# Performance work log

Measured on AMD Instinct MI355X. Metric: run time of the kernel, lower is better.

## Reference

```python
import jax, jax.numpy as jnp
import numpy as np

B, O, R, I, D = 256, 10, 1152, 8, 16
NUM_ITERATIONS = 3


def squash(x, axis=-1):
    sq = jnp.sum(x * x, axis=axis, keepdims=True)
    return (sq / (1.0 + sq)) * x / jnp.sqrt(sq)


def setup_inputs() -> dict:
    key = jax.random.key(0)
    k1, k2 = jax.random.split(key)
    inputs = jax.random.normal(k1, (B, R, I), dtype=jnp.float32)
    route_weights = jax.random.normal(k2, (O, R, I, D), dtype=jnp.float32)
    return {"inputs": inputs, "route_weights": route_weights}


def reference(inputs, route_weights):
    # priors: [B, O, R, D]  (torch keeps an extra singleton dim: [B,O,R,1,D])
    priors = jnp.einsum('bri,orid->bord', inputs, route_weights)
    logits = jnp.zeros_like(priors)  # torch initializes logits with priors' shape
    outputs = None
    for _ in range(NUM_ITERATIONS):
        probs = jax.nn.softmax(logits, axis=2)  # softmax over route nodes (dim=2)
        outputs = squash(jnp.sum(probs * priors, axis=2, keepdims=True))  # [B,O,1,D]
        delta = jnp.sum(priors * outputs, axis=-1, keepdims=True)  # [B,O,R,1]
        logits = logits + delta  # broadcasts over vec dim, as in torch
    return outputs  # [B, O, 1, D]
```

## Files before the change

### kernel.cpp

```cpp
#include <hip/hip_runtime.h>


#define BB 256
#define OO 10
#define RR 1152
#define DD 16
#define NITER 3
#define NT 384
#define NB 2
#define GRID (OO * BB / NB)
#define NW 6

template<int CTRL>
__device__ __forceinline__ float dpp_add(float x) {
    int p = __builtin_amdgcn_update_dpp(0, __float_as_int(x), CTRL, 0xF, 0xF, true);
    return x + __int_as_float(p);
}
__device__ __forceinline__ float red_dq(float x) {
    x = dpp_add<0xB1>(x);
    x = dpp_add<0x4E>(x);
    return x;
}
__device__ __forceinline__ float4 fma4(float4 w, float a, float4 c) {
    c.x = fmaf(w.x, a, c.x); c.y = fmaf(w.y, a, c.y);
    c.z = fmaf(w.z, a, c.z); c.w = fmaf(w.w, a, c.w);
    return c;
}
__device__ __forceinline__ float dot4(float4 a, float4 b) {
    return fmaf(a.x, b.x, fmaf(a.y, b.y, fmaf(a.z, b.z, a.w * b.w)));
}
__device__ __forceinline__ float red_rs(float x) {
    x += __shfl_xor(x, 4);  x += __shfl_xor(x, 8);
    x += __shfl_xor(x, 16); x += __shfl_xor(x, 32);
    return x;
}
__device__ __forceinline__ float4 red_rs4(float4 v) {
    v.x = red_rs(v.x); v.y = red_rs(v.y); v.z = red_rs(v.z); v.w = red_rs(v.w);
    return v;
}

struct F4x4 { float4 q0, q1, q2, q3; };

__global__ void capsule_direct(
    const float* __restrict__ inp,
    const float* __restrict__ W,
    float* __restrict__ out)
{
    __shared__ float4 priB[12 * NT];
    __shared__ float4 red4[NB][NW][4];
    __shared__ float  redS[NB][NW];
    __shared__ __align__(16) float finalv[NB][20];

    int wg = blockIdx.x;
    wg = (wg & 7) * (GRID / 8) + (wg >> 3);
    const int o  = wg / (BB / NB);
    const int b0 = (wg % (BB / NB)) * NB;
    const int tid = threadIdx.x;
    const int dq = tid & 3;
    const int rslot = tid >> 2;
    const int wid = tid >> 6;
    const int lane = tid & 63;

    const float4* w4 = reinterpret_cast<const float4*>(W) + (size_t)o * (RR * 32) + dq;
    const float4* ip = reinterpret_cast<const float4*>(inp);

    F4x4 PAa{}, PAb{}, PAc{};
    float4 lgAa{0,0,0,0}, lgAb{0,0,0,0}, lgAc{0,0,0,0};
    float4 lgBa{0,0,0,0}, lgBb{0,0,0,0}, lgBc{0,0,0,0};

#define DO_C(C, PACC) do {                                                     \
        const int row_ = (C) * 96 + rslot;                                     \
        const float4 a0_ = ip[((size_t)b0 * RR + row_) * 2];                   \
        const float4 a1_ = ip[((size_t)b0 * RR + row_) * 2 + 1];               \
        const float4 c0_ = ip[((size_t)(b0 + 1) * RR + row_) * 2];             \
        const float4 c1_ = ip[((size_t)(b0 + 1) * RR + row_) * 2 + 1];         \
        const float4* wr_ = w4 + row_ * 32;                                    \
        float4 pb_{0.f, 0.f, 0.f, 0.f};                                        \
        float4 w_;                                                             \
        w_ = wr_[0];  PACC = fma4(w_, a0_.x, PACC); pb_ = fma4(w_, c0_.x, pb_);\
        w_ = wr_[4];  PACC = fma4(w_, a0_.y, PACC); pb_ = fma4(w_, c0_.y, pb_);\
        w_ = wr_[8];  PACC = fma4(w_, a0_.z, PACC); pb_ = fma4(w_, c0_.z, pb_);\
        w_ = wr_[12]; PACC = fma4(w_, a0_.w, PACC); pb_ = fma4(w_, c0_.w, pb_);\
        w_ = wr_[16]; PACC = fma4(w_, a1_.x, PACC); pb_ = fma4(w_, c1_.x, pb_);\
        w_ = wr_[20]; PACC = fma4(w_, a1_.y, PACC); pb_ = fma4(w_, c1_.y, pb_);\
        w_ = wr_[24]; PACC = fma4(w_, a1_.z, PACC); pb_ = fma4(w_, c1_.z, pb_);\
        w_ = wr_[28]; PACC = fma4(w_, a1_.w, PACC); pb_ = fma4(w_, c1_.w, pb_);\
        priB[(C) * NT + tid] = pb_;                                            \
    } while (0)

    DO_C(0,  PAa.q0); DO_C(1,  PAa.q1); DO_C(2,  PAa.q2); DO_C(3,  PAa.q3);
    DO_C(4,  PAb.q0); DO_C(5,  PAb.q1); DO_C(6,  PAb.q2); DO_C(7,  PAb.q3);
    DO_C(8,  PAc.q0); DO_C(9,  PAc.q1); DO_C(10, PAc.q2); DO_C(11, PAc.q3);

    #pragma unroll
    for (int it = 0; it < NITER; ++it) {
        {
            float4 ea, eb, ec;
            ea.x = __expf(lgAa.x); ea.y = __expf(lgAa.y);
            ea.z = __expf(lgAa.z); ea.w = __expf(lgAa.w);
            eb.x = __expf(lgAb.x); eb.y = __expf(lgAb.y);
            eb.z = __expf(lgAb.z); eb.w = __expf(lgAb.w);
            ec.x = __expf(lgAc.x); ec.y = __expf(lgAc.y);
            ec.z = __expf(lgAc.z); ec.w = __expf(lgAc.w);
            float Se = ea.x + ea.y + ea.z + ea.w + eb.x + eb.y + eb.z + eb.w
                     + ec.x + ec.y + ec.z + ec.w;
            float4 s4{0.f, 0.f, 0.f, 0.f};
            s4 = fma4(PAa.q0, ea.x, s4); s4 = fma4(PAa.q1, ea.y, s4);
            s4 = fma4(PAa.q2, ea.z, s4); s4 = fma4(PAa.q3, ea.w, s4);
            s4 = fma4(PAb.q0, eb.x, s4); s4 = fma4(PAb.q1, eb.y, s4);
            s4 = fma4(PAb.q2, eb.z, s4); s4 = fma4(PAb.q3, eb.w, s4);
            s4 = fma4(PAc.q0, ec.x, s4); s4 = fma4(PAc.q1, ec.y, s4);
            s4 = fma4(PAc.q2, ec.z, s4); s4 = fma4(PAc.q3, ec.w, s4);
            s4 = red_rs4(s4);
            Se = red_rs(Se);
            if (lane < 4) red4[0][wid][lane] = s4;
            else if (lane == 4) redS[0][wid] = Se;
        }
        {
            float4 ea, eb, ec;
            ea.x = __expf(lgBa.x); ea.y = __expf(lgBa.y);
            ea.z = __expf(lgBa.z); ea.w = __expf(lgBa.w);
            eb.x = __expf(lgBb.x); eb.y = __expf(lgBb.y);
            eb.z = __expf(lgBb.z); eb.w = __expf(lgBb.w);
            ec.x = __expf(lgBc.x); ec.y = __expf(lgBc.y);
            ec.z = __expf(lgBc.z); ec.w = __expf(lgBc.w);
            float Se = ea.x + ea.y + ea.z + ea.w + eb.x + eb.y + eb.z + eb.w
                     + ec.x + ec.y + ec.z + ec.w;
            float4 s4{0.f, 0.f, 0.f, 0.f};
            s4 = fma4(priB[0  * NT + tid], ea.x, s4);
            s4 = fma4(priB[1  * NT + tid], ea.y, s4);
            s4 = fma4(priB[2  * NT + tid], ea.z, s4);
            s4 = fma4(priB[3  * NT + tid], ea.w, s4);
            s4 = fma4(priB[4  * NT + tid], eb.x, s4);
            s4 = fma4(priB[5  * NT + tid], eb.y, s4);
            s4 = fma4(priB[6  * NT + tid], eb.z, s4);
            s4 = fma4(priB[7  * NT + tid], eb.w, s4);
            s4 = fma4(priB[8  * NT + tid], ec.x, s4);
            s4 = fma4(priB[9  * NT + tid], ec.y, s4);
            s4 = fma4(priB[10 * NT + tid], ec.z, s4);
            s4 = fma4(priB[11 * NT + tid], ec.w, s4);
            s4 = red_rs4(s4);
            Se = red_rs(Se);
            if (lane < 4) red4[1][wid][lane] = s4;
            else if (lane == 4) redS[1][wid] = Se;
        }
        __syncthreads();

        if (tid < 34) {
            const int nb = (tid >= 17) ? 1 : 0;
            const int j = tid - nb * 17;
            float t = 0.f;
            if (j < 16) {
                const float* base = (const float*)red4 + nb * (NW * 16) + j;
                #pragma unroll
                for (int w = 0; w < NW; ++w) t += base[w * 16];
            } else {
                #pragma unroll
                for (int w = 0; w < NW; ++w) t += redS[nb][w];
            }
            finalv[nb][j] = t;
        }
        __syncthreads();

        {
            const float4* fp = reinterpret_cast<const float4*>(&finalv[0][0]);
            const float4 f0 = fp[0], f1 = fp[1], f2 = fp[2], f3 = fp[3];
            const float S = finalv[0][16];
            const float inv = 1.0f / S;
            const float sq = (dot4(f0, f0) + dot4(f1, f1) + dot4(f2, f2)
                              + dot4(f3, f3)) * inv * inv;
            const float F = inv * sqrtf(sq) / (1.0f + sq);
            if (it < NITER - 1) {
                const float4 vq = fp[dq];
                lgAa.x = fmaf(F, red_dq(dot4(PAa.q0, vq)), lgAa.x);
                lgAa.y = fmaf(F, red_dq(dot4(PAa.q1, vq)), lgAa.y);
                lgAa.z = fmaf(F, red_dq(dot4(PAa.q2, vq)), lgAa.z);
                lgAa.w = fmaf(F, red_dq(dot4(PAa.q3, vq)), lgAa.w);
                lgAb.x = fmaf(F, red_dq(dot4(PAb.q0, vq)), lgAb.x);
                lgAb.y = fmaf(F, red_dq(dot4(PAb.q1, vq)), lgAb.y);
                lgAb.z = fmaf(F, red_dq(dot4(PAb.q2, vq)), lgAb.z);
                lgAb.w = fmaf(F, red_dq(dot4(PAb.q3, vq)), lgAb.w);
                lgAc.x = fmaf(F, red_dq(dot4(PAc.q0, vq)), lgAc.x);
                lgAc.y = fmaf(F, red_dq(dot4(PAc.q1, vq)), lgAc.y);
                lgAc.z = fmaf(F, red_dq(dot4(PAc.q2, vq)), lgAc.z);
                lgAc.w = fmaf(F, red_dq(dot4(PAc.q3, vq)), lgAc.w);
            } else if (tid < DD) {
                out[((size_t)b0 * OO + o) * DD + tid] = finalv[0][tid] * F;
            }
        }
        {
            const float4* fp = reinterpret_cast<const float4*>(&finalv[1][0]);
            const float4 f0 = fp[0], f1 = fp[1], f2 = fp[2], f3 = fp[3];
            const float S = finalv[1][16];
            const float inv = 1.0f / S;
            const float sq = (dot4(f0, f0) + dot4(f1, f1) + dot4(f2, f2)
                              + dot4(f3, f3)) * inv * inv;
            const float F = inv * sqrtf(sq) / (1.0f + sq);
            if (it < NITER - 1) {
                const float4 vq = fp[dq];
                lgBa.x = fmaf(F, red_dq(dot4(priB[0  * NT + tid], vq)), lgBa.x);
                lgBa.y = fmaf(F, red_dq(dot4(priB[1  * NT + tid], vq)), lgBa.y);
                lgBa.z = fmaf(F, red_dq(dot4(priB[2  * NT + tid], vq)), lgBa.z);
                lgBa.w = fmaf(F, red_dq(dot4(priB[3  * NT + tid], vq)), lgBa.w);
                lgBb.x = fmaf(F, red_dq(dot4(priB[4  * NT + tid], vq)), lgBb.x);
                lgBb.y = fmaf(F, red_dq(dot4(priB[5  * NT + tid], vq)), lgBb.y);
                lgBb.z = fmaf(F, red_dq(dot4(priB[6  * NT + tid], vq)), lgBb.z);
                lgBb.w = fmaf(F, red_dq(dot4(priB[7  * NT + tid], vq)), lgBb.w);
                lgBc.x = fmaf(F, red_dq(dot4(priB[8  * NT + tid], vq)), lgBc.x);
                lgBc.y = fmaf(F, red_dq(dot4(priB[9  * NT + tid], vq)), lgBc.y);
                lgBc.z = fmaf(F, red_dq(dot4(priB[10 * NT + tid], vq)), lgBc.z);
                lgBc.w = fmaf(F, red_dq(dot4(priB[11 * NT + tid], vq)), lgBc.w);
            } else if (tid < DD) {
                out[((size_t)(b0 + 1) * OO + o) * DD + tid] = finalv[1][tid] * F;
            }
        }
    }
}

extern "C" void kernel_launch(void* const* d_in, const int* in_sizes, int n_in,
                              void* d_out, int out_size, void* d_ws, size_t ws_size,
                              hipStream_t stream) {
    const float* inputs = (const float*)d_in[0];
    const float* W = (const float*)d_in[1];
    float* out = (float*)d_out;
    hipLaunchKernelGGL(capsule_direct, dim3(GRID), dim3(NT), 0, stream,
                       inputs, W, out);
}
```

Baseline: 153.8 us.

## Process one batch element per workgroup instead of two, dropping LDS prior buffer

Each workgroup now handles a single (o, b) pair, so the grid doubles and the second batch element's priors no longer need to be staged in a 72KB shared-memory buffer. This removes LDS traffic and the LDS occupancy limit, allowing more workgroups per CU. The cost is that each weight row is loaded from global/L2 once per batch element instead of being shared across two, doubling weight read traffic. A launch bound is also added.

```diff
diff --git a/kernel.cpp b/kernel.cpp
--- a/kernel.cpp
+++ b/kernel.cpp
@@ -7,8 +7,7 @@
 #define DD 16
 #define NITER 3
 #define NT 384
-#define NB 2
-#define GRID (OO * BB / NB)
+#define GRID (OO * BB)
 #define NW 6
 
 template<int CTRL>
@@ -41,177 +40,116 @@
 
 struct F4x4 { float4 q0, q1, q2, q3; };
 
-__global__ void capsule_direct(
+__global__ __launch_bounds__(NT) void capsule_nb1(
     const float* __restrict__ inp,
     const float* __restrict__ W,
     float* __restrict__ out)
 {
-    __shared__ float4 priB[12 * NT];
-    __shared__ float4 red4[NB][NW][4];
-    __shared__ float  redS[NB][NW];
-    __shared__ __align__(16) float finalv[NB][20];
+    __shared__ float4 red4[NW][4];
+    __shared__ float  redS[NW];
+    __shared__ __align__(16) float finalv[20];
 
     int wg = blockIdx.x;
     wg = (wg & 7) * (GRID / 8) + (wg >> 3);
-    const int o  = wg / (BB / NB);
-    const int b0 = (wg % (BB / NB)) * NB;
+    const int o = wg / BB;
+    const int b = wg % BB;
     const int tid = threadIdx.x;
     const int dq = tid & 3;
     const int rslot = tid >> 2;
     const int wid = tid >> 6;
     const int lane = tid & 63;
 
-    const float4* w4 = reinterpret_cast<const float4*>(W) + (size_t)o * (RR * 32) + dq;
-    const float4* ip = reinterpret_cast<const float4*>(inp);
+    const float4* w4 = reinterpret_cast<const float4*>(W)
+                       + (size_t)o * (RR * 32) + dq;
+    const float4* ip = reinterpret_cast<const float4*>(inp) + (size_t)b * (RR * 2);
 
-    F4x4 PAa{}, PAb{}, PAc{};
-    float4 lgAa{0,0,0,0}, lgAb{0,0,0,0}, lgAc{0,0,0,0};
-    float4 lgBa{0,0,0,0}, lgBb{0,0,0,0}, lgBc{0,0,0,0};
+    F4x4 Pa{}, Pb{}, Pc{};
+    float4 lga{0,0,0,0}, lgb{0,0,0,0}, lgc{0,0,0,0};
 
 #define DO_C(C, PACC) do {                                                     \
         const int row_ = (C) * 96 + rslot;                                     \
-        const float4 a0_ = ip[((size_t)b0 * RR + row_) * 2];                   \
-        const float4 a1_ = ip[((size_t)b0 * RR + row_) * 2 + 1];               \
-        const float4 c0_ = ip[((size_t)(b0 + 1) * RR + row_) * 2];             \
-        const float4 c1_ = ip[((size_t)(b0 + 1) * RR + row_) * 2 + 1];         \
+        const float4 a0_ = ip[row_ * 2];                                       \
+        const float4 a1_ = ip[row_ * 2 + 1];                                   \
         const float4* wr_ = w4 + row_ * 32;                                    \
-        float4 pb_{0.f, 0.f, 0.f, 0.f};                                        \
         float4 w_;                                                             \
-        w_ = wr_[0];  PACC = fma4(w_, a0_.x, PACC); pb_ = fma4(w_, c0_.x, pb_);\
-        w_ = wr_[4];  PACC = fma4(w_, a0_.y, PACC); pb_ = fma4(w_, c0_.y, pb_);\
-        w_ = wr_[8];  PACC = fma4(w_, a0_.z, PACC); pb_ = fma4(w_, c0_.z, pb_);\
-        w_ = wr_[12]; PACC = fma4(w_, a0_.w, PACC); pb_ = fma4(w_, c0_.w, pb_);\
-        w_ = wr_[16]; PACC = fma4(w_, a1_.x, PACC); pb_ = fma4(w_, c1_.x, pb_);\
-        w_ = wr_[20]; PACC = fma4(w_, a1_.y, PACC); pb_ = fma4(w_, c1_.y, pb_);\
-        w_ = wr_[24]; PACC = fma4(w_, a1_.z, PACC); pb_ = fma4(w_, c1_.z, pb_);\
-        w_ = wr_[28]; PACC = fma4(w_, a1_.w, PACC); pb_ = fma4(w_, c1_.w, pb_);\
-        priB[(C) * NT + tid] = pb_;                                            \
+        w_ = wr_[0];  PACC = fma4(w_, a0_.x, PACC);                            \
+        w_ = wr_[4];  PACC = fma4(w_, a0_.y, PACC);                            \
+        w_ = wr_[8];  PACC = fma4(w_, a0_.z, PACC);                            \
+        w_ = wr_[12]; PACC = fma4(w_, a0_.w, PACC);                            \
+        w_ = wr_[16]; PACC = fma4(w_, a1_.x, PACC);                            \
+        w_ = wr_[20]; PACC = fma4(w_, a1_.y, PACC);                            \
+        w_ = wr_[24]; PACC = fma4(w_, a1_.z, PACC);                            \
+        w_ = wr_[28]; PACC = fma4(w_, a1_.w, PACC);                            \
     } while (0)
 
-    DO_C(0,  PAa.q0); DO_C(1,  PAa.q1); DO_C(2,  PAa.q2); DO_C(3,  PAa.q3);
-    DO_C(4,  PAb.q0); DO_C(5,  PAb.q1); DO_C(6,  PAb.q2); DO_C(7,  PAb.q3);
-    DO_C(8,  PAc.q0); DO_C(9,  PAc.q1); DO_C(10, PAc.q2); DO_C(11, PAc.q3);
+    DO_C(0,  Pa.q0); DO_C(1,  Pa.q1); DO_C(2,  Pa.q2); DO_C(3,  Pa.q3);
+    DO_C(4,  Pb.q0); DO_C(5,  Pb.q1); DO_C(6,  Pb.q2); DO_C(7,  Pb.q3);
+    DO_C(8,  Pc.q0); DO_C(9,  Pc.q1); DO_C(10, Pc.q2); DO_C(11, Pc.q3);
 
     #pragma unroll
     for (int it = 0; it < NITER; ++it) {
         {
             float4 ea, eb, ec;
-            ea.x = __expf(lgAa.x); ea.y = __expf(lgAa.y);
-            ea.z = __expf(lgAa.z); ea.w = __expf(lgAa.w);
-            eb.x = __expf(lgAb.x); eb.y = __expf(lgAb.y);
-            eb.z = __expf(lgAb.z); eb.w = __expf(lgAb.w);
-            ec.x = __expf(lgAc.x); ec.y = __expf(lgAc.y);
-            ec.z = __expf(lgAc.z); ec.w = __expf(lgAc.w);
+            ea.x = __expf(lga.x); ea.y = __expf(lga.y);
+            ea.z = __expf(lga.z); ea.w = __expf(lga.w);
+            eb.x = __expf(lgb.x); eb.y = __expf(lgb.y);
+            eb.z = __expf(lgb.z); eb.w = __expf(lgb.w);
+            ec.x = __expf(lgc.x); ec.y = __expf(lgc.y);
+            ec.z = __expf(lgc.z); ec.w = __expf(lgc.w);
             float Se = ea.x + ea.y + ea.z + ea.w + eb.x + eb.y + eb.z + eb.w
                      + ec.x + ec.y + ec.z + ec.w;
             float4 s4{0.f, 0.f, 0.f, 0.f};
-            s4 = fma4(PAa.q0, ea.x, s4); s4 = fma4(PAa.q1, ea.y, s4);
-            s4 = fma4(PAa.q2, ea.z, s4); s4 = fma4(PAa.q3, ea.w, s4);
-            s4 = fma4(PAb.q0, eb.x, s4); s4 = fma4(PAb.q1, eb.y, s4);
-            s4 = fma4(PAb.q2, eb.z, s4); s4 = fma4(PAb.q3, eb.w, s4);
-            s4 = fma4(PAc.q0, ec.x, s4); s4 = fma4(PAc.q1, ec.y, s4);
-            s4 = fma4(PAc.q2, ec.z, s4); s4 = fma4(PAc.q3, ec.w, s4);
+            s4 = fma4(Pa.q0, ea.x, s4); s4 = fma4(Pa.q1, ea.y, s4);
+            s4 = fma4(Pa.q2, ea.z, s4); s4 = fma4(Pa.q3, ea.w, s4);
+            s4 = fma4(Pb.q0, eb.x, s4); s4 = fma4(Pb.q1, eb.y, s4);
+            s4 = fma4(Pb.q2, eb.z, s4); s4 = fma4(Pb.q3, eb.w, s4);
+            s4 = fma4(Pc.q0, ec.x, s4); s4 = fma4(Pc.q1, ec.y, s4);
+            s4 = fma4(Pc.q2, ec.z, s4); s4 = fma4(Pc.q3, ec.w, s4);
             s4 = red_rs4(s4);
             Se = red_rs(Se);
-            if (lane < 4) red4[0][wid][lane] = s4;
-            else if (lane == 4) redS[0][wid] = Se;
-        }
-        {
-            float4 ea, eb, ec;
-            ea.x = __expf(lgBa.x); ea.y = __expf(lgBa.y);
-            ea.z = __expf(lgBa.z); ea.w = __expf(lgBa.w);
-            eb.x = __expf(lgBb.x); eb.y = __expf(lgBb.y);
-            eb.z = __expf(lgBb.z); eb.w = __expf(lgBb.w);
-            ec.x = __expf(lgBc.x); ec.y = __expf(lgBc.y);
-            ec.z = __expf(lgBc.z); ec.w = __expf(lgBc.w);
-            float Se = ea.x + ea.y + ea.z + ea.w + eb.x + eb.y + eb.z + eb.w
-                     + ec.x + ec.y + ec.z + ec.w;
-            float4 s4{0.f, 0.f, 0.f, 0.f};
-            s4 = fma4(priB[0  * NT + tid], ea.x, s4);
-            s4 = fma4(priB[1  * NT + tid], ea.y, s4);
-            s4 = fma4(priB[2  * NT + tid], ea.z, s4);
-            s4 = fma4(priB[3  * NT + tid], ea.w, s4);
-            s4 = fma4(priB[4  * NT + tid], eb.x, s4);
-            s4 = fma4(priB[5  * NT + tid], eb.y, s4);
-            s4 = fma4(priB[6  * NT + tid], eb.z, s4);
-            s4 = fma4(priB[7  * NT + tid], eb.w, s4);
-            s4 = fma4(priB[8  * NT + tid], ec.x, s4);
-            s4 = fma4(priB[9  * NT + tid], ec.y, s4);
-            s4 = fma4(priB[10 * NT + tid], ec.z, s4);
-            s4 = fma4(priB[11 * NT + tid], ec.w, s4);
-            s4 = red_rs4(s4);
-            Se = red_rs(Se);
-            if (lane < 4) red4[1][wid][lane] = s4;
-            else if (lane == 4) redS[1][wid] = Se;
+            if (lane < 4) red4[wid][lane] = s4;
+            else if (lane == 4) redS[wid] = Se;
         }
         __syncthreads();
 
-        if (tid < 34) {
-            const int nb = (tid >= 17) ? 1 : 0;
-            const int j = tid - nb * 17;
+        if (tid < 17) {
             float t = 0.f;
-            if (j < 16) {
-                const float* base = (const float*)red4 + nb * (NW * 16) + j;
+            if (tid < 16) {
+                const float* base = (const float*)red4 + tid;
                 #pragma unroll
                 for (int w = 0; w < NW; ++w) t += base[w * 16];
             } else {
                 #pragma unroll
-                for (int w = 0; w < NW; ++w) t += redS[nb][w];
+                for (int w = 0; w < NW; ++w) t += redS[w];
             }
-            finalv[nb][j] = t;
+            finalv[tid] = t;
         }
         __syncthreads();
 
         {
-            const float4* fp = reinterpret_cast<const float4*>(&finalv[0][0]);
+            const float4* fp = reinterpret_cast<const float4*>(&finalv[0]);
             const float4 f0 = fp[0], f1 = fp[1], f2 = fp[2], f3 = fp[3];
-            const float S = finalv[0][16];
+            const float S = finalv[16];
             const float inv = 1.0f / S;
             const float sq = (dot4(f0, f0) + dot4(f1, f1) + dot4(f2, f2)
                               + dot4(f3, f3)) * inv * inv;
             const float F = inv * sqrtf(sq) / (1.0f + sq);
             if (it < NITER - 1) {
                 const float4 vq = fp[dq];
-                lgAa.x = fmaf(F, red_dq(dot4(PAa.q0, vq)), lgAa.x);
-                lgAa.y = fmaf(F, red_dq(dot4(PAa.q1, vq)), lgAa.y);
-                lgAa.z = fmaf(F, red_dq(dot4(PAa.q2, vq)), lgAa.z);
-                lgAa.w = fmaf(F, red_dq(dot4(PAa.q3, vq)), lgAa.w);
-                lgAb.x = fmaf(F, red_dq(dot4(PAb.q0, vq)), lgAb.x);
-                lgAb.y = fmaf(F, red_dq(dot4(PAb.q1, vq)), lgAb.y);
-                lgAb.z = fmaf(F, red_dq(dot4(PAb.q2, vq)), lgAb.z);
-                lgAb.w = fmaf(F, red_dq(dot4(PAb.q3, vq)), lgAb.w);
-                lgAc.x = fmaf(F, red_dq(dot4(PAc.q0, vq)), lgAc.x);
-                lgAc.y = fmaf(F, red_dq(dot4(PAc.q1, vq)), lgAc.y);
-                lgAc.z = fmaf(F, red_dq(dot4(PAc.q2, vq)), lgAc.z);
-                lgAc.w = fmaf(F, red_dq(dot4(PAc.q3, vq)), lgAc.w);
+                lga.x = fmaf(F, red_dq(dot4(Pa.q0, vq)), lga.x);
+                lga.y = fmaf(F, red_dq(dot4(Pa.q1, vq)), lga.y);
+                lga.z = fmaf(F, red_dq(dot4(Pa.q2, vq)), lga.z);
+                lga.w = fmaf(F, red_dq(dot4(Pa.q3, vq)), lga.w);
+                lgb.x = fmaf(F, red_dq(dot4(Pb.q0, vq)), lgb.x);
+                lgb.y = fmaf(F, red_dq(dot4(Pb.q1, vq)), lgb.y);
+                lgb.z = fmaf(F, red_dq(dot4(Pb.q2, vq)), lgb.z);
+                lgb.w = fmaf(F, red_dq(dot4(Pb.q3, vq)), lgb.w);
+                lgc.x = fmaf(F, red_dq(dot4(Pc.q0, vq)), lgc.x);
+                lgc.y = fmaf(F, red_dq(dot4(Pc.q1, vq)), lgc.y);
+                lgc.z = fmaf(F, red_dq(dot4(Pc.q2, vq)), lgc.z);
+                lgc.w = fmaf(F, red_dq(dot4(Pc.q3, vq)), lgc.w);
             } else if (tid < DD) {
-                out[((size_t)b0 * OO + o) * DD + tid] = finalv[0][tid] * F;
-            }
-        }
-        {
-            const float4* fp = reinterpret_cast<const float4*>(&finalv[1][0]);
-            const float4 f0 = fp[0], f1 = fp[1], f2 = fp[2], f3 = fp[3];
-            const float S = finalv[1][16];
-            const float inv = 1.0f / S;
-            const float sq = (dot4(f0, f0) + dot4(f1, f1) + dot4(f2, f2)
-                              + dot4(f3, f3)) * inv * inv;
-            const float F = inv * sqrtf(sq) / (1.0f + sq);
-            if (it < NITER - 1) {
-                const float4 vq = fp[dq];
-                lgBa.x = fmaf(F, red_dq(dot4(priB[0  * NT + tid], vq)), lgBa.x);
-                lgBa.y = fmaf(F, red_dq(dot4(priB[1  * NT + tid], vq)), lgBa.y);
-                lgBa.z = fmaf(F, red_dq(dot4(priB[2  * NT + tid], vq)), lgBa.z);
-                lgBa.w = fmaf(F, red_dq(dot4(priB[3  * NT + tid], vq)), lgBa.w);
-                lgBb.x = fmaf(F, red_dq(dot4(priB[4  * NT + tid], vq)), lgBb.x);
-                lgBb.y = fmaf(F, red_dq(dot4(priB[5  * NT + tid], vq)), lgBb.y);
-                lgBb.z = fmaf(F, red_dq(dot4(priB[6  * NT + tid], vq)), lgBb.z);
-                lgBb.w = fmaf(F, red_dq(dot4(priB[7  * NT + tid], vq)), lgBb.w);
-                lgBc.x = fmaf(F, red_dq(dot4(priB[8  * NT + tid], vq)), lgBc.x);
-                lgBc.y = fmaf(F, red_dq(dot4(priB[9  * NT + tid], vq)), lgBc.y);
-                lgBc.z = fmaf(F, red_dq(dot4(priB[10 * NT + tid], vq)), lgBc.z);
-                lgBc.w = fmaf(F, red_dq(dot4(priB[11 * NT + tid], vq)), lgBc.w);
-            } else if (tid < DD) {
-                out[((size_t)(b0 + 1) * OO + o) * DD + tid] = finalv[1][tid] * F;
+                out[((size_t)b * OO + o) * DD + tid] = finalv[tid] * F;
             }
         }
     }
@@ -223,6 +161,6 @@
     const float* inputs = (const float*)d_in[0];
     const float* W = (const float*)d_in[1];
     float* out = (float*)d_out;
-    hipLaunchKernelGGL(capsule_direct, dim3(GRID), dim3(NT), 0, stream,
+    hipLaunchKernelGGL(capsule_nb1, dim3(GRID), dim3(NT), 0, stream,
                        inputs, W, out);
 }
```

After: 152.1 us. No clear change (-1.1%).
